# Optimization experiments

Hardware: AMD Instinct MI355X
Metric: run time of the kernel (lower is better)

The kernel has to match this reference:

```python
import jax, jax.numpy as jnp
import numpy as np

B, P, C = 4, 2048, 1024
N_HEADS = 16
HEAD = C // N_HEADS


def setup_inputs() -> dict:
    key = jax.random.key(0)
    ks = jax.random.split(key, 9)
    s = C ** -0.5
    return {
        "x": jax.random.normal(ks[0], (B, P, C), dtype=jnp.float32),
        "Wq": jax.random.normal(ks[1], (C, C), dtype=jnp.float32) * s,
        "bq": jnp.zeros((C,), dtype=jnp.float32),
        "Wk": jax.random.normal(ks[2], (C, C), dtype=jnp.float32) * s,
        "bk": jnp.zeros((C,), dtype=jnp.float32),
        "Wv": jax.random.normal(ks[3], (C, C), dtype=jnp.float32) * s,
        "bv": jnp.zeros((C,), dtype=jnp.float32),
        "Wo": jax.random.normal(ks[4], (C, C), dtype=jnp.float32) * s,
        "bo": jnp.zeros((C,), dtype=jnp.float32),
    }


def _attn(x, Wq, bq, Wk, bk, Wv, bv, Wo, bo):
    b, p, c = x.shape
    q = (x @ Wq + bq).reshape(b, p, N_HEADS, HEAD).transpose(0, 2, 1, 3)
    k = (x @ Wk + bk).reshape(b, p, N_HEADS, HEAD).transpose(0, 2, 1, 3)
    v = (x @ Wv + bv).reshape(b, p, N_HEADS, HEAD).transpose(0, 2, 1, 3)
    # scores: [B, H, P, P]
    w = jnp.einsum('bhqd,bhkd->bhqk', q, k) * (HEAD ** -0.5)
    w = jax.nn.softmax(w, axis=-1)
    y = jnp.einsum('bhqk,bhkd->bhqd', w, v)
    y = y.transpose(0, 2, 1, 3).reshape(b, p, c)
    return y @ Wo + bo


def reference(x, Wq, bq, Wk, bk, Wv, bv, Wo, bo):
    return _attn(x, Wq, bq, Wk, bk, Wv, bv, Wo, bo)
```

## Files before the change

kernel.cpp:

```cpp
#include <hip/hip_runtime.h>

#define B_DIM 4
#define P_DIM 2048
#define C_DIM 1024
#define H_CNT 16
#define D_HEAD 64
#define M_DIM 8192
#define K_DIM 1024

typedef __attribute__((ext_vector_type(4))) float  f32x4;
typedef __attribute__((ext_vector_type(8))) __bf16 bf16x8;
typedef __attribute__((ext_vector_type(4))) __bf16 bf16x4;
typedef __attribute__((ext_vector_type(4))) short  s16x4;
typedef __attribute__((ext_vector_type(8))) short  s16x8;

static __device__ __forceinline__ short f2bf(float f) {
    unsigned u = __float_as_uint(f);
    u += 0x7fff + ((u >> 16) & 1);
    return (short)(u >> 16);
}

#define GLDS16(src, dst) __builtin_amdgcn_global_load_lds( \
    (__attribute__((address_space(1))) void*)(void*)(src), \
    (__attribute__((address_space(3))) void*)(void*)(dst), 16, 0, 0)

__global__ __launch_bounds__(256) void cvt_f32_bf16(const float* __restrict__ in,
                                                    short* __restrict__ out) {
    size_t i = ((size_t)blockIdx.x * 256 + threadIdx.x) * 4;
    f32x4 v = *(const f32x4*)(in + i);
    s16x4 o;
    o[0] = f2bf(v[0]); o[1] = f2bf(v[1]); o[2] = f2bf(v[2]); o[3] = f2bf(v[3]);
    *(s16x4*)(out + i) = o;
}

__global__ __launch_bounds__(256) void wtrans_all(const float* __restrict__ W0,
                                                  const float* __restrict__ W1,
                                                  const float* __restrict__ W2,
                                                  const float* __restrict__ W3,
                                                  short* __restrict__ WT) {
    __shared__ float t[32][33];
    const int z = blockIdx.z;
    const float* W = z == 0 ? W0 : z == 1 ? W1 : z == 2 ? W2 : W3;
    short* dst = WT + (size_t)z * C_DIM * C_DIM;
    const int k0 = blockIdx.y * 32, n0 = blockIdx.x * 32;
    const int tx = threadIdx.x & 31, ty = threadIdx.x >> 5;
#pragma unroll
    for (int j = 0; j < 4; ++j)
        t[ty + j * 8][tx] = W[(size_t)(k0 + ty + j * 8) * C_DIM + n0 + tx];
    __syncthreads();
#pragma unroll
    for (int j = 0; j < 4; ++j)
        dst[(size_t)(n0 + ty + j * 8) * C_DIM + k0 + tx] = f2bf(t[tx][ty + j * 8]);
}

template<int MODE>
__global__ __launch_bounds__(256) void gemm_bt(const short* __restrict__ A,
                                               const short* __restrict__ BT,
                                               const float* __restrict__ bias,
                                               const float* __restrict__ bias2,
                                               const float* __restrict__ bias3,
                                               void* __restrict__ outp,
                                               float scale) {
    __shared__ __align__(16) short lA[128 * 32];
    __shared__ __align__(16) short lB[128 * 32];
    const int tid = threadIdx.x;
    const int lane = tid & 63;
    const int w = tid >> 6;
    const int m0 = blockIdx.y * 128;
    const int n0 = blockIdx.x * 128;
    const int wr = (w >> 1) * 64;
    const int wc = (w & 1) * 64;
    const int li = lane & 15, g = lane >> 4;

    f32x4 acc[4][4] = {};

    const int r0s = tid >> 2, r1s = (tid + 256) >> 2;
    const int c0 = (tid & 3) ^ ((r0s >> 1) & 3);
    const int c1 = (tid & 3) ^ ((r1s >> 1) & 3);
    const short* a0 = A + (size_t)(m0 + r0s) * K_DIM + c0 * 8;
    const short* a1 = A + (size_t)(m0 + r1s) * K_DIM + c1 * 8;
    const short* b0 = BT + (size_t)(n0 + r0s) * K_DIM + c0 * 8;
    const short* b1 = BT + (size_t)(n0 + r1s) * K_DIM + c1 * 8;
    short* lA0 = lA + w * 512;  short* lA1 = lA + 2048 + w * 512;
    short* lB0 = lB + w * 512;  short* lB1 = lB + 2048 + w * 512;

    int aoff[4], boff[4];
#pragma unroll
    for (int i = 0; i < 4; ++i) {
        int ra = wr + i * 16 + li;  int pa = g ^ ((ra >> 1) & 3);
        aoff[i] = ra * 32 + pa * 8;
        int rb = wc + i * 16 + li;  int pb = g ^ ((rb >> 1) & 3);
        boff[i] = rb * 32 + pb * 8;
    }

    for (int k0 = 0; k0 < K_DIM; k0 += 32) {
        __syncthreads();
        GLDS16(a0 + k0, lA0);
        GLDS16(a1 + k0, lA1);
        GLDS16(b0 + k0, lB0);
        GLDS16(b1 + k0, lB1);
        __syncthreads();
        bf16x8 af[4], bfr[4];
#pragma unroll
        for (int i = 0; i < 4; ++i) {
            af[i]  = *(const bf16x8*)&lA[aoff[i]];
            bfr[i] = *(const bf16x8*)&lB[boff[i]];
        }
#pragma unroll
        for (int i = 0; i < 4; ++i)
#pragma unroll
            for (int j = 0; j < 4; ++j)
                acc[i][j] = __builtin_amdgcn_mfma_f32_16x16x32_bf16(
                    af[i], bfr[j], acc[i][j], 0, 0, 0);
    }

#pragma unroll
    for (int j = 0; j < 4; ++j) {
        const int nn = n0 + wc + j * 16 + li;
        const float* bp = bias; int bidx = nn; float sc = scale;
        if (MODE == 3) {
            bp = nn < 1024 ? bias : (nn < 2048 ? bias2 : bias3);
            bidx = nn & 1023;
            sc = nn < 1024 ? scale : 1.0f;
        }
        const float bb = bp[bidx];
#pragma unroll
        for (int i = 0; i < 4; ++i) {
#pragma unroll
            for (int r = 0; r < 4; ++r) {
                const int mm = m0 + wr + i * 16 + 4 * g + r;
                float val = (acc[i][j][r] + bb) * sc;
                if (MODE == 1) {
                    ((float*)outp)[(size_t)mm * C_DIM + nn] = val;
                } else {
                    const int bI = mm >> 11, p = mm & 2047;
                    const int proj = nn >> 10, hI = (nn >> 6) & 15, d = nn & 63;
                    short* base = (short*)outp + (size_t)proj * M_DIM * C_DIM;
                    if (proj < 2)
                        base[(((size_t)bI * H_CNT + hI) * P_DIM + p) * D_HEAD + d] = f2bf(val);
                    else
                        base[(((size_t)bI * H_CNT + hI) * D_HEAD + d) * P_DIM + p] = f2bf(val);
                }
            }
        }
    }
}

__global__ __launch_bounds__(256, 2) void attn_fwd(const short* __restrict__ Q,
                                                   const short* __restrict__ Kb,
                                                   const short* __restrict__ VT,
                                                   short* __restrict__ Y) {
    const int bh = blockIdx.y;
    const int b = bh >> 4, h = bh & 15;
    const int tid = threadIdx.x;
    const int w = tid >> 6, lane = tid & 63;
    const int li = lane & 15, g = lane >> 4;
    const int x7 = li & 7;
    const int q0 = blockIdx.x * 128 + w * 32;
    const short* Qh = Q + (size_t)bh * P_DIM * D_HEAD;
    const short* Kh = Kb + (size_t)bh * P_DIM * D_HEAD;
    const short* Vh = VT + (size_t)bh * D_HEAD * P_DIM;

    __shared__ __align__(16) short lK[64 * 64];
    __shared__ __align__(16) short lV[64 * 64];
    __shared__ __align__(16) short pb[4][32 * 64];
    short* pw = pb[w];

    bf16x8 qf[2][2];
#pragma unroll
    for (int qt = 0; qt < 2; ++qt)
#pragma unroll
        for (int c = 0; c < 2; ++c)
            qf[qt][c] = *(const bf16x8*)&Qh[(size_t)(q0 + qt * 16 + li) * D_HEAD + c * 32 + g * 8];

    f32x4 o[2][4] = {};
    float ps[2] = {};

    const int t1 = tid + 256;
    const int r0 = tid >> 3, u0 = (tid & 7) ^ (r0 & 7);
    const int r1 = t1 >> 3,  u1 = (t1 & 7) ^ (r1 & 7);
    const short* ks0 = Kh + r0 * D_HEAD + u0 * 8;
    const short* ks1 = Kh + r1 * D_HEAD + u1 * 8;
    const short* vs0 = Vh + r0 * P_DIM + u0 * 8;
    const short* vs1 = Vh + r1 * P_DIM + u1 * 8;
    short* dk0 = lK + tid * 8;  short* dk1 = lK + t1 * 8;
    short* dv0 = lV + tid * 8;  short* dv1 = lV + t1 * 8;

    const int pwrow0 = li * 64;
    const int wsw = x7 << 1;

    for (int k0 = 0; k0 < P_DIM; k0 += 64) {
        __syncthreads();
        GLDS16(ks0 + (size_t)k0 * D_HEAD, dk0);
        GLDS16(ks1 + (size_t)k0 * D_HEAD, dk1);
        GLDS16(vs0 + k0, dv0);
        GLDS16(vs1 + k0, dv1);
        __syncthreads();

        bf16x8 kf[4][2];
#pragma unroll
        for (int kt = 0; kt < 4; ++kt) {
            const int rbase = (kt * 16 + li) * 64;
            kf[kt][0] = *(const bf16x8*)&lK[rbase + ((0 + g) ^ x7) * 8];
            kf[kt][1] = *(const bf16x8*)&lK[rbase + ((4 + g) ^ x7) * 8];
        }

#pragma unroll
        for (int qt = 0; qt < 2; ++qt) {
            f32x4 s[4] = {};
#pragma unroll
            for (int kt = 0; kt < 4; ++kt) {
                s[kt] = __builtin_amdgcn_mfma_f32_16x16x32_bf16(kf[kt][0], qf[qt][0], s[kt], 0, 0, 0);
                s[kt] = __builtin_amdgcn_mfma_f32_16x16x32_bf16(kf[kt][1], qf[qt][1], s[kt], 0, 0, 0);
            }
            const int rowb = pwrow0 + qt * 16 * 64;
#pragma unroll
            for (int kt = 0; kt < 4; ++kt) {
                bf16x4 pv4;
#pragma unroll
                for (int r = 0; r < 4; ++r) {
                    float e = __expf(s[kt][r]);
                    ps[qt] += e;
                    pv4[r] = (__bf16)e;
                }
                const int j = (kt * 4 + g) ^ wsw;
                *(bf16x4*)&pw[rowb + j * 4] = pv4;
            }
        }
        __builtin_amdgcn_sched_barrier(0);
        asm volatile("s_waitcnt lgkmcnt(0)" ::: "memory");
        __builtin_amdgcn_sched_barrier(0);
#pragma unroll
        for (int kc = 0; kc < 2; ++kc) {
            bf16x8 pf[2];
#pragma unroll
            for (int qt = 0; qt < 2; ++qt) {
                const int j = (8 * kc + 2 * g) ^ wsw;
                pf[qt] = *(const bf16x8*)&pw[(qt * 16 + li) * 64 + j * 4];
            }
#pragma unroll
            for (int dt = 0; dt < 4; ++dt) {
                bf16x8 vf = *(const bf16x8*)&lV[(dt * 16 + li) * 64 + ((kc * 4 + g) ^ x7) * 8];
                o[0][dt] = __builtin_amdgcn_mfma_f32_16x16x32_bf16(pf[0], vf, o[0][dt], 0, 0, 0);
                o[1][dt] = __builtin_amdgcn_mfma_f32_16x16x32_bf16(pf[1], vf, o[1][dt], 0, 0, 0);
            }
        }
    }

#pragma unroll
    for (int qt = 0; qt < 2; ++qt) {
        float v = ps[qt];
        v += __shfl_xor(v, 16);
        v += __shfl_xor(v, 32);
#pragma unroll
        for (int r = 0; r < 4; ++r) {
            const float inv = 1.0f / __shfl(v, 4 * g + r);
            const int p = q0 + qt * 16 + 4 * g + r;
            short* yrow = Y + ((size_t)b * P_DIM + p) * C_DIM + h * D_HEAD;
#pragma unroll
            for (int dt = 0; dt < 4; ++dt)
                yrow[dt * 16 + li] = f2bf(o[qt][dt][r] * inv);
        }
    }
}

extern "C" void kernel_launch(void* const* d_in, const int* in_sizes, int n_in,
                              void* d_out, int out_size, void* d_ws, size_t ws_size,
                              hipStream_t stream) {
    (void)in_sizes; (void)n_in; (void)out_size; (void)ws_size;
    const float* x  = (const float*)d_in[0];
    const float* Wq = (const float*)d_in[1];
    const float* bq = (const float*)d_in[2];
    const float* Wk = (const float*)d_in[3];
    const float* bk = (const float*)d_in[4];
    const float* Wv = (const float*)d_in[5];
    const float* bv = (const float*)d_in[6];
    const float* Wo = (const float*)d_in[7];
    const float* bo = (const float*)d_in[8];

    short* ws  = (short*)d_ws;
    short* xb  = ws;
    short* wqt = xb  + (size_t)M_DIM * C_DIM;
    short* wot = wqt + 3 * (size_t)C_DIM * C_DIM;
    short* qd  = wot + (size_t)C_DIM * C_DIM;
    short* kd  = qd  + (size_t)M_DIM * C_DIM;
    short* vtd = kd  + (size_t)M_DIM * C_DIM;
    short* yd  = vtd + (size_t)M_DIM * C_DIM;

    cvt_f32_bf16<<<dim3(M_DIM * C_DIM / 1024), 256, 0, stream>>>(x, xb);
    wtrans_all<<<dim3(32, 32, 4), 256, 0, stream>>>(Wq, Wk, Wv, Wo, wqt);
    gemm_bt<3><<<dim3(24, 64), 256, 0, stream>>>(xb, wqt, bq, bk, bv, (void*)qd, 0.125f);
    attn_fwd<<<dim3(16, 64), 256, 0, stream>>>(qd, kd, vtd, yd);
    gemm_bt<1><<<dim3(8, 64), 256, 0, stream>>>(yd, wot, bo, nullptr, nullptr, d_out, 1.0f);
}
```

Baseline: 212.4 us.

## Vectorize GEMM epilogue stores via operand swap, split V projection, add block swizzle

The GEMM now swaps MFMA operands for the Q/K and output projections, so each lane holds four consecutive columns and can write packed 4-wide bf16 or float4 stores instead of scattered scalar stores. The V projection moves to its own launch, which keeps the original operand order so that its transposed output is also written as packed 4-element runs along P. A block-index remap spreads neighbouring blocks across different M rows, intended to improve L2 reuse. The price is one extra kernel launch and the loss of the single fused QKV grid.

```diff
diff --git a/kernel.cpp b/kernel.cpp
--- a/kernel.cpp
+++ b/kernel.cpp
@@ -58,16 +58,19 @@
                                                const short* __restrict__ BT,
                                                const float* __restrict__ bias,
                                                const float* __restrict__ bias2,
-                                               const float* __restrict__ bias3,
                                                void* __restrict__ outp,
-                                               float scale) {
+                                               int gx) {
+    const int h = blockIdx.y * gx + blockIdx.x;
+    const int cpx = (gx << 6) >> 3;
+    const int lid = (h & 7) * cpx + (h >> 3);
+    const int m0 = (lid / gx) * 128;
+    const int n0 = (lid % gx) * 128;
+
     __shared__ __align__(16) short lA[128 * 32];
     __shared__ __align__(16) short lB[128 * 32];
     const int tid = threadIdx.x;
     const int lane = tid & 63;
     const int w = tid >> 6;
-    const int m0 = blockIdx.y * 128;
-    const int n0 = blockIdx.x * 128;
     const int wr = (w >> 1) * 64;
     const int wc = (w & 1) * 64;
     const int li = lane & 15, g = lane >> 4;
@@ -109,38 +112,63 @@
 #pragma unroll
         for (int i = 0; i < 4; ++i)
 #pragma unroll
-            for (int j = 0; j < 4; ++j)
-                acc[i][j] = __builtin_amdgcn_mfma_f32_16x16x32_bf16(
-                    af[i], bfr[j], acc[i][j], 0, 0, 0);
-    }
-
-#pragma unroll
-    for (int j = 0; j < 4; ++j) {
-        const int nn = n0 + wc + j * 16 + li;
-        const float* bp = bias; int bidx = nn; float sc = scale;
-        if (MODE == 3) {
-            bp = nn < 1024 ? bias : (nn < 2048 ? bias2 : bias3);
-            bidx = nn & 1023;
-            sc = nn < 1024 ? scale : 1.0f;
-        }
-        const float bb = bp[bidx];
-#pragma unroll
-        for (int i = 0; i < 4; ++i) {
-#pragma unroll
-            for (int r = 0; r < 4; ++r) {
-                const int mm = m0 + wr + i * 16 + 4 * g + r;
-                float val = (acc[i][j][r] + bb) * sc;
-                if (MODE == 1) {
-                    ((float*)outp)[(size_t)mm * C_DIM + nn] = val;
-                } else {
-                    const int bI = mm >> 11, p = mm & 2047;
-                    const int proj = nn >> 10, hI = (nn >> 6) & 15, d = nn & 63;
-                    short* base = (short*)outp + (size_t)proj * M_DIM * C_DIM;
-                    if (proj < 2)
-                        base[(((size_t)bI * H_CNT + hI) * P_DIM + p) * D_HEAD + d] = f2bf(val);
-                    else
-                        base[(((size_t)bI * H_CNT + hI) * D_HEAD + d) * P_DIM + p] = f2bf(val);
-                }
+            for (int j = 0; j < 4; ++j) {
+                if (MODE == 2)
+                    acc[i][j] = __builtin_amdgcn_mfma_f32_16x16x32_bf16(
+                        af[i], bfr[j], acc[i][j], 0, 0, 0);
+                else
+                    acc[i][j] = __builtin_amdgcn_mfma_f32_16x16x32_bf16(
+                        bfr[j], af[i], acc[i][j], 0, 0, 0);
+            }
+    }
+
+    if (MODE == 0) {
+#pragma unroll
+        for (int j = 0; j < 4; ++j) {
+            const int nb = n0 + wc + j * 16 + 4 * g;
+            const float* bp = nb < 1024 ? bias : bias2;
+            const float sc = nb < 1024 ? 0.125f : 1.0f;
+            const f32x4 bb = *(const f32x4*)&bp[nb & 1023];
+            const int hI = (nb >> 6) & 15, d = nb & 63;
+            short* base = (short*)outp + (size_t)(nb >> 10) * M_DIM * C_DIM;
+#pragma unroll
+            for (int i = 0; i < 4; ++i) {
+                const int m = m0 + wr + i * 16 + li;
+                const int bI = m >> 11, p = m & 2047;
+                s16x4 v4;
+#pragma unroll
+                for (int r = 0; r < 4; ++r) v4[r] = f2bf((acc[i][j][r] + bb[r]) * sc);
+                *(s16x4*)&base[(((size_t)bI * H_CNT + hI) * P_DIM + p) * D_HEAD + d] = v4;
+            }
+        }
+    } else if (MODE == 1) {
+#pragma unroll
+        for (int j = 0; j < 4; ++j) {
+            const int nb = n0 + wc + j * 16 + 4 * g;
+            const f32x4 bb = *(const f32x4*)&bias[nb];
+#pragma unroll
+            for (int i = 0; i < 4; ++i) {
+                const int m = m0 + wr + i * 16 + li;
+                f32x4 v;
+#pragma unroll
+                for (int r = 0; r < 4; ++r) v[r] = acc[i][j][r] + bb[r];
+                *(f32x4*)&((float*)outp)[(size_t)m * C_DIM + nb] = v;
+            }
+        }
+    } else {
+#pragma unroll
+        for (int j = 0; j < 4; ++j) {
+            const int nn = n0 + wc + j * 16 + li;
+            const float bb = bias[nn];
+            const int hI = nn >> 6, d = nn & 63;
+#pragma unroll
+            for (int i = 0; i < 4; ++i) {
+                const int pbse = m0 + wr + i * 16 + 4 * g;
+                const int bI = pbse >> 11, p = pbse & 2047;
+                s16x4 v4;
+#pragma unroll
+                for (int r = 0; r < 4; ++r) v4[r] = f2bf(acc[i][j][r] + bb);
+                *(s16x4*)&((short*)outp)[(((size_t)bI * H_CNT + hI) * D_HEAD + d) * P_DIM + p] = v4;
             }
         }
     }
@@ -281,15 +309,18 @@
     short* ws  = (short*)d_ws;
     short* xb  = ws;
     short* wqt = xb  + (size_t)M_DIM * C_DIM;
+    short* wvt = wqt + 2 * (size_t)C_DIM * C_DIM;
     short* wot = wqt + 3 * (size_t)C_DIM * C_DIM;
     short* qd  = wot + (size_t)C_DIM * C_DIM;
     short* kd  = qd  + (size_t)M_DIM * C_DIM;
     short* vtd = kd  + (size_t)M_DIM * C_DIM;
     short* yd  = vtd + (size_t)M_DIM * C_DIM;
+    (void)kd;
 
     cvt_f32_bf16<<<dim3(M_DIM * C_DIM / 1024), 256, 0, stream>>>(x, xb);
     wtrans_all<<<dim3(32, 32, 4), 256, 0, stream>>>(Wq, Wk, Wv, Wo, wqt);
-    gemm_bt<3><<<dim3(24, 64), 256, 0, stream>>>(xb, wqt, bq, bk, bv, (void*)qd, 0.125f);
+    gemm_bt<0><<<dim3(16, 64), 256, 0, stream>>>(xb, wqt, bq, bk, (void*)qd, 16);
+    gemm_bt<2><<<dim3(8, 64), 256, 0, stream>>>(xb, wvt, bv, nullptr, (void*)vtd, 8);
     attn_fwd<<<dim3(16, 64), 256, 0, stream>>>(qd, kd, vtd, yd);
-    gemm_bt<1><<<dim3(8, 64), 256, 0, stream>>>(yd, wot, bo, nullptr, nullptr, d_out, 1.0f);
-}
+    gemm_bt<1><<<dim3(8, 64), 256, 0, stream>>>(yd, wot, bo, nullptr, d_out, 8);
+}
```

After: 204.5 us. -3.7%, faster.
